# Kernel optimization log

Hardware: AMD Instinct MI355X
Metric: run time of the kernel (lower is better)

The kernel has to match this reference:

```python
import math
import jax, jax.numpy as jnp
import numpy as np

B, C, F, W_FRAMES = 1, 8, 1024, 512
H = 16                      # num_heads
D = F // H                  # head dim = 64
ROPE_DIM = D // 2           # 32: only first half of head dim is rotated
EXP = 4                     # ffn expansion
EPS = 1e-5
MAX_FREQ = 10.0             # rotary-embedding-torch default


def frame_norm(x, g, b):
    # LayerNorm over the feature axis (axis=2) of (b, c, F, w)
    mu = jnp.mean(x, axis=2, keepdims=True)
    var = jnp.mean(jnp.square(x - mu), axis=2, keepdims=True)
    xn = (x - mu) * jax.lax.rsqrt(var + EPS)
    return xn * g[None, None, :, None] + b[None, None, :, None]


def mc_linear(x, w_pw):
    # per-channel pointwise linear: out[b,c,f,w] = sum_g W[c,f,g] x[b,c,g,w]
    return jnp.einsum('bcgw,cfg->bcfw', x, w_pw)


def apply_rope(t, freqs_seq):
    # t: (b, c, H, w, d); freqs_seq: (w, rot_dim)
    rot_dim = freqs_seq.shape[-1]
    t_rot, t_pass = t[..., :rot_dim], t[..., rot_dim:]
    cos, sin = jnp.cos(freqs_seq), jnp.sin(freqs_seq)
    x1, x2 = t_rot[..., 0::2], t_rot[..., 1::2]
    rh = jnp.stack([-x2, x1], axis=-1).reshape(t_rot.shape)  # interleaved rotate_half
    return jnp.concatenate([t_rot * cos + rh * sin, t_pass], axis=-1)


def attention(x, w_q, w_o, rope_freqs):
    b, c, f, w = x.shape
    # NOTE: source uses q_proj for q, k AND v (k_proj/v_proj unused)
    p = mc_linear(x, w_q)                                    # (b,c,F,w)
    t = p.transpose(0, 1, 3, 2).reshape(b, c, w, H, D).transpose(0, 1, 3, 2, 4)  # (b,c,H,w,d)
    pos = jnp.arange(w, dtype=t.dtype)
    freqs_seq = jnp.repeat(pos[:, None] * rope_freqs[None, :], 2, axis=-1)  # (w, rot_dim)
    q = apply_rope(t, freqs_seq)
    k = apply_rope(t, freqs_seq)
    v = t
    scores = jnp.einsum('bchqd,bchkd->bchqk', q, k) / math.sqrt(f)  # scaled by sqrt(features)!
    a = jax.nn.softmax(scores, axis=-1)
    o = jnp.einsum('bchqk,bchkd->bchqd', a, v)
    o = o.transpose(0, 1, 3, 2, 4).reshape(b, c, w, f).transpose(0, 1, 3, 2)  # (b,c,F,w)
    return mc_linear(o, w_o)


def setup_inputs() -> dict:
    key = jax.random.key(0)
    ks = jax.random.split(key, 8)
    s = 1.0 / math.sqrt(F)
    se = 1.0 / math.sqrt(F * EXP)
    x = jax.random.normal(ks[0], (B, C, F, W_FRAMES), dtype=jnp.float32)
    w_q = jax.random.uniform(ks[1], (C, F, F), jnp.float32, -s, s)
    w_o = jax.random.uniform(ks[2], (C, F, F), jnp.float32, -s, s)
    w1 = jax.random.uniform(ks[3], (C, F * EXP, F), jnp.float32, -s, s)
    w2 = jax.random.uniform(ks[4], (C, F, F * EXP), jnp.float32, -se, se)
    rope_freqs = jnp.linspace(1.0, MAX_FREQ / 2, ROPE_DIM // 2, dtype=jnp.float32) * math.pi
    return {
        'x': x,
        'norm1_g': jnp.ones((F,), jnp.float32), 'norm1_b': jnp.zeros((F,), jnp.float32),
        'w_q': w_q, 'w_o': w_o, 'rope_freqs': rope_freqs,
        'norm2_g': jnp.ones((F,), jnp.float32), 'norm2_b': jnp.zeros((F,), jnp.float32),
        'w1': w1, 'w2': w2,
    }


def reference(x, norm1_g, norm1_b, w_q, w_o, rope_freqs, norm2_g, norm2_b, w1, w2):
    # FrameTransformerEncoder, eval mode (dropout = identity)
    z = frame_norm(x, norm1_g, norm1_b)
    x = x + attention(z, w_q, w_o, rope_freqs)
    z = frame_norm(x, norm2_g, norm2_b)
    z = mc_linear(jax.nn.gelu(mc_linear(z, w1), approximate=False), w2)
    return x + z
```

## Files before the change

kernel.cpp:

```cpp
#include <hip/hip_runtime.h>
#include <math.h>

#define CC 8
#define FF 1024
#define WW 512
#define HH 16
#define DD 64
#define FE 4096
#define EPS_ 1e-5f

typedef __attribute__((ext_vector_type(8))) short bf16x8;
typedef __attribute__((ext_vector_type(4))) float f32x4;

static __device__ __forceinline__ unsigned short f2bf(float f) {
    unsigned u = __float_as_uint(f);
    u += 0x7fffu + ((u >> 16) & 1u);
    return (unsigned short)(u >> 16);
}
static __device__ __forceinline__ float bf2f(unsigned short h) {
    return __uint_as_float(((unsigned)h) << 16);
}
static __device__ __forceinline__ float gelu_exact(float v) {
    return 0.5f * v * (1.0f + erff(v * 0.70710678118654752f));
}

typedef const __attribute__((address_space(1))) unsigned int* gas_p;
typedef __attribute__((address_space(3))) unsigned int* las_p;
static __device__ __forceinline__ void gload_lds16(const void* g, void* l) {
    __builtin_amdgcn_global_load_lds((gas_p)g, (las_p)l, 16, 0, 0);
}

__global__ __launch_bounds__(256) void fn_stats_k(
    const float* __restrict__ x, float2* __restrict__ part)
{
    int c  = blockIdx.z;
    int w0 = blockIdx.x * 64;
    int f0 = blockIdx.y * 128;
    int t  = threadIdx.x, wl = t & 63, fg = t >> 6;
    const float* xc = x + (size_t)c * FF * WW;

    float s = 0.f, q = 0.f;
    #pragma unroll 8
    for (int i = 0; i < 32; i++) {
        int f = f0 + fg + 4 * i;
        float v = xc[(size_t)f * WW + w0 + wl];
        s += v; q += v * v;
    }
    __shared__ float ss[4][64], sq_[4][64];
    ss[fg][wl] = s; sq_[fg][wl] = q;
    __syncthreads();
    if (fg == 0) {
        float S = 0.f, Q = 0.f;
        #pragma unroll
        for (int j = 0; j < 4; j++) { S += ss[j][wl]; Q += sq_[j][wl]; }
        part[((size_t)c * WW + w0 + wl) * 8 + blockIdx.y] = make_float2(S, Q);
    }
}

__global__ __launch_bounds__(256) void fn_apply_k(
    const float* __restrict__ x, const float2* __restrict__ part,
    const float* __restrict__ g, const float* __restrict__ b,
    unsigned short* __restrict__ zt)
{
    int c  = blockIdx.z;
    int w0 = blockIdx.x * 64;
    int f0 = blockIdx.y * 64;
    int t  = threadIdx.x, wl = t & 63, fg = t >> 6;

    __shared__ float smu[64], srv[64];
    __shared__ float sT[64][65];

    if (t < 64) {
        float S = 0.f, Q = 0.f;
        #pragma unroll
        for (int fs = 0; fs < 8; fs++) {
            float2 v = part[((size_t)c * WW + w0 + t) * 8 + fs];
            S += v.x; Q += v.y;
        }
        float mu  = S * (1.f / FF);
        float var = Q * (1.f / FF) - mu * mu;
        smu[t] = mu;
        srv[t] = rsqrtf(var + EPS_);
    }
    const float* xc = x + (size_t)c * FF * WW;
    #pragma unroll
    for (int i = 0; i < 16; i++) {
        int fl = fg * 16 + i;
        sT[fl][wl] = xc[(size_t)(f0 + fl) * WW + w0 + wl];
    }
    __syncthreads();

    unsigned short* ztc = zt + (size_t)c * WW * FF;
    float gv = g[f0 + wl], bv = b[f0 + wl];
    #pragma unroll
    for (int i = 0; i < 16; i++) {
        int wr = fg * 16 + i;
        ztc[(size_t)(w0 + wr) * FF + f0 + wl] =
            f2bf((sT[wl][wr] - smu[wr]) * srv[wr] * gv + bv);
    }
}

__global__ __launch_bounds__(256, 3) void gemm_v3_k(
    const float* __restrict__ A, const unsigned short* __restrict__ Bt,
    float* __restrict__ Outf, unsigned short* __restrict__ Outb,
    const float* __restrict__ Add, int M, int K, int mode)
{
    int bid = blockIdx.x;
    int c   = bid & 7;
    int rem = bid >> 3;
    int nt  = rem & 3;
    int mt  = rem >> 2;
    int m0  = mt * 64, n0 = nt * 128;
    const float*          Ac = A  + (size_t)c * M * K;
    const unsigned short* Bc = Bt + ((size_t)c * 512 + n0) * K;

    __shared__ unsigned short sA[2][64 * 72];
    __shared__ unsigned short sB[2][128 * 64];

    int t    = threadIdx.x;
    int lane = t & 63;
    int wid  = t >> 6;
    int frl  = lane & 15, fgr = lane >> 4;
    int WM   = (wid >> 1) * 32, WN = (wid & 1) * 64;

    f32x4 acc[2][4];
    #pragma unroll
    for (int i = 0; i < 2; i++)
        #pragma unroll
        for (int j = 0; j < 4; j++) acc[i][j] = (f32x4){0.f, 0.f, 0.f, 0.f};

    int arow = t >> 4;
    int acol = (t & 15) * 4;
    float4 ar[4];

    int bro   = lane >> 3;
    int bslot = (lane & 7) ^ bro;

    auto loadA = [&](int k0) {
        #pragma unroll
        for (int p = 0; p < 4; p++)
            ar[p] = *reinterpret_cast<const float4*>(
                Ac + (size_t)(m0 + p * 16 + arow) * K + k0 + acol);
    };
    auto writeA = [&](int buf) {
        #pragma unroll
        for (int p = 0; p < 4; p++) {
            ushort4 h;
            h.x = f2bf(ar[p].x); h.y = f2bf(ar[p].y);
            h.z = f2bf(ar[p].z); h.w = f2bf(ar[p].w);
            *reinterpret_cast<ushort4*>(&sA[buf][(p * 16 + arow) * 72 + acol]) = h;
        }
    };
    auto stageB = [&](int buf, int k0) {
        #pragma unroll
        for (int r = 0; r < 4; r++) {
            int rbase = wid * 32 + r * 8;
            gload_lds16(Bc + (size_t)(rbase + bro) * K + k0 + bslot * 8,
                        &sB[buf][rbase * 64]);
        }
    };

    loadA(0);
    stageB(0, 0);
    writeA(0);
    __syncthreads();

    int NT = K >> 6;
    for (int kt = 0; kt < NT; ++kt) {
        int cur = kt & 1;
        if (kt + 1 < NT) {
            loadA((kt + 1) << 6);
            stageB(cur ^ 1, (kt + 1) << 6);
        }
        #pragma unroll
        for (int ks = 0; ks < 2; ks++) {
            bf16x8 af[2], bfv[4];
            #pragma unroll
            for (int mi = 0; mi < 2; mi++)
                af[mi] = *reinterpret_cast<const bf16x8*>(
                    &sA[cur][(WM + mi * 16 + frl) * 72 + ks * 32 + fgr * 8]);
            #pragma unroll
            for (int ni = 0; ni < 4; ni++) {
                int row  = WN + ni * 16 + frl;
                int slot = ((ks << 2) | fgr) ^ (frl & 7);
                bfv[ni] = *reinterpret_cast<const bf16x8*>(
                    &sB[cur][row * 64 + slot * 8]);
            }
            #pragma unroll
            for (int mi = 0; mi < 2; mi++)
                #pragma unroll
                for (int ni = 0; ni < 4; ni++)
                    acc[mi][ni] = __builtin_amdgcn_mfma_f32_16x16x32_bf16(
                        af[mi], bfv[ni], acc[mi][ni], 0, 0, 0);
        }
        if (kt + 1 < NT) writeA(cur ^ 1);
        __syncthreads();
    }

    if (mode == 1) {
        #pragma unroll
        for (int mi = 0; mi < 2; mi++)
            #pragma unroll
            for (int ni = 0; ni < 4; ni++) {
                int mrow = m0 + WM + mi * 16 + fgr * 4;
                int ncol = n0 + WN + ni * 16 + frl;
                #pragma unroll
                for (int r = 0; r < 4; r++) {
                    size_t o = ((size_t)c * M + mrow + r) * 512 + ncol;
                    Outf[o] = acc[mi][ni][r] + Add[o];
                }
            }
    } else {
        bool gel = (mode == 2);
        #pragma unroll
        for (int mi = 0; mi < 2; mi++)
            #pragma unroll
            for (int ni = 0; ni < 4; ni++) {
                f32x4 v = acc[mi][ni];
                if (gel) {
                    v[0] = gelu_exact(v[0]); v[1] = gelu_exact(v[1]);
                    v[2] = gelu_exact(v[2]); v[3] = gelu_exact(v[3]);
                }
                int mrow = m0 + WM + mi * 16 + fgr * 4;
                int ncol = n0 + WN + ni * 16 + frl;
                ushort4 h;
                h.x = f2bf(v[0]); h.y = f2bf(v[1]);
                h.z = f2bf(v[2]); h.w = f2bf(v[3]);
                *reinterpret_cast<ushort4*>(
                    &Outb[((size_t)c * 512 + ncol) * M + mrow]) = h;
            }
    }
}

__global__ __launch_bounds__(256) void attn_mfma_k(
    const unsigned short* __restrict__ pt, const float* __restrict__ fr,
    unsigned short* __restrict__ ot)
{
    int ch = blockIdx.y;
    int c  = ch >> 4, h = ch & 15;
    int q0 = blockIdx.x * 64;
    int t  = threadIdx.x;
    int lane = t & 63;
    int wid  = t >> 6;
    int frl  = lane & 15, fgr = lane >> 4;

    const unsigned short* base = pt + (size_t)c * WW * FF + h * DD;

    __shared__ unsigned short Qs[64 * 72];
    __shared__ unsigned short Ks[64 * 72];
    __shared__ unsigned short Vt[64 * 72];
    __shared__ unsigned short Ps[4 * 16 * 72];

    {
        int kr = t >> 3, d0 = (t & 7) * 8;
        #pragma unroll
        for (int r = 0; r < 2; r++) {
            int row = kr + r * 32;
            int w   = q0 + row;
            bf16x8 v = *reinterpret_cast<const bf16x8*>(&base[(size_t)w * FF + d0]);
            bf16x8 o;
            if (d0 < 32) {
                #pragma unroll
                for (int j = 0; j < 8; j += 2) {
                    float x1 = bf2f((unsigned short)v[j]);
                    float x2 = bf2f((unsigned short)v[j + 1]);
                    float sn, cs;
                    __sincosf((float)w * fr[(d0 + j) >> 1], &sn, &cs);
                    o[j]     = (short)f2bf(x1 * cs - x2 * sn);
                    o[j + 1] = (short)f2bf(x2 * cs + x1 * sn);
                }
            } else o = v;
            *reinterpret_cast<bf16x8*>(&Qs[row * 72 + d0]) = o;
        }
    }

    f32x4 oacc[4];
    float m_[4], l_[4];
    #pragma unroll
    for (int i = 0; i < 4; i++) {
        oacc[i] = (f32x4){0.f, 0.f, 0.f, 0.f};
        m_[i] = -1e30f; l_[i] = 0.f;
    }
    unsigned short* myP = &Ps[wid * 16 * 72];
    int wq0 = wid * 16;

    for (int k0 = 0; k0 < WW; k0 += 64) {
        __syncthreads();
        {
            int kr = t >> 3, d0 = (t & 7) * 8;
            #pragma unroll
            for (int r = 0; r < 2; r++) {
                int row = kr + r * 32;
                int w   = k0 + row;
                bf16x8 v = *reinterpret_cast<const bf16x8*>(&base[(size_t)w * FF + d0]);
                bf16x8 o;
                if (d0 < 32) {
                    #pragma unroll
                    for (int j = 0; j < 8; j += 2) {
                        float x1 = bf2f((unsigned short)v[j]);
                        float x2 = bf2f((unsigned short)v[j + 1]);
                        float sn, cs;
                        __sincosf((float)w * fr[(d0 + j) >> 1], &sn, &cs);
                        o[j]     = (short)f2bf(x1 * cs - x2 * sn);
                        o[j + 1] = (short)f2bf(x2 * cs + x1 * sn);
                    }
                } else o = v;
                *reinterpret_cast<bf16x8*>(&Ks[row * 72 + d0]) = o;
            }
        }
        {
            int d  = t & 63;
            int kb = (t >> 6) * 8;
            #pragma unroll
            for (int r = 0; r < 2; r++) {
                int kk = kb + r * 32;
                bf16x8 o;
                #pragma unroll
                for (int j = 0; j < 8; j++)
                    o[j] = (short)base[(size_t)(k0 + kk + j) * FF + d];
                *reinterpret_cast<bf16x8*>(&Vt[d * 72 + kk]) = o;
            }
        }
        __syncthreads();

        f32x4 s[4];
        #pragma unroll
        for (int nt = 0; nt < 4; nt++) s[nt] = (f32x4){0.f, 0.f, 0.f, 0.f};
        bf16x8 aq0 = *reinterpret_cast<const bf16x8*>(&Qs[(wq0 + frl) * 72 + fgr * 8]);
        bf16x8 aq1 = *reinterpret_cast<const bf16x8*>(&Qs[(wq0 + frl) * 72 + 32 + fgr * 8]);
        #pragma unroll
        for (int nt = 0; nt < 4; nt++) {
            bf16x8 b0 = *reinterpret_cast<const bf16x8*>(&Ks[(nt * 16 + frl) * 72 + fgr * 8]);
            bf16x8 b1 = *reinterpret_cast<const bf16x8*>(&Ks[(nt * 16 + frl) * 72 + 32 + fgr * 8]);
            s[nt] = __builtin_amdgcn_mfma_f32_16x16x32_bf16(aq0, b0, s[nt], 0, 0, 0);
            s[nt] = __builtin_amdgcn_mfma_f32_16x16x32_bf16(aq1, b1, s[nt], 0, 0, 0);
        }

        #pragma unroll
        for (int r = 0; r < 4; r++) {
            float sv[4];
            #pragma unroll
            for (int nt = 0; nt < 4; nt++) sv[nt] = s[nt][r] * (1.f / 32.f);
            float mx = fmaxf(fmaxf(sv[0], sv[1]), fmaxf(sv[2], sv[3]));
            mx = fmaxf(mx, __shfl_xor(mx, 1, 64));
            mx = fmaxf(mx, __shfl_xor(mx, 2, 64));
            mx = fmaxf(mx, __shfl_xor(mx, 4, 64));
            mx = fmaxf(mx, __shfl_xor(mx, 8, 64));
            float mn    = fmaxf(m_[r], mx);
            float scale = __expf(m_[r] - mn);
            float rs = 0.f;
            #pragma unroll
            for (int nt = 0; nt < 4; nt++) {
                float p = __expf(sv[nt] - mn);
                myP[(fgr * 4 + r) * 72 + nt * 16 + frl] = f2bf(p);
                rs += p;
            }
            rs += __shfl_xor(rs, 1, 64);
            rs += __shfl_xor(rs, 2, 64);
            rs += __shfl_xor(rs, 4, 64);
            rs += __shfl_xor(rs, 8, 64);
            l_[r] = l_[r] * scale + rs;
            m_[r] = mn;
            #pragma unroll
            for (int dt = 0; dt < 4; dt++) oacc[dt][r] *= scale;
        }

        bf16x8 ap0 = *reinterpret_cast<const bf16x8*>(&myP[frl * 72 + fgr * 8]);
        bf16x8 ap1 = *reinterpret_cast<const bf16x8*>(&myP[frl * 72 + 32 + fgr * 8]);
        #pragma unroll
        for (int dt = 0; dt < 4; dt++) {
            bf16x8 b0 = *reinterpret_cast<const bf16x8*>(&Vt[(dt * 16 + frl) * 72 + fgr * 8]);
            bf16x8 b1 = *reinterpret_cast<const bf16x8*>(&Vt[(dt * 16 + frl) * 72 + 32 + fgr * 8]);
            oacc[dt] = __builtin_amdgcn_mfma_f32_16x16x32_bf16(ap0, b0, oacc[dt], 0, 0, 0);
            oacc[dt] = __builtin_amdgcn_mfma_f32_16x16x32_bf16(ap1, b1, oacc[dt], 0, 0, 0);
        }
    }

    unsigned short* ob = ot + (size_t)c * WW * FF + h * DD;
    #pragma unroll
    for (int r = 0; r < 4; r++) {
        float inv = 1.f / l_[r];
        int w = q0 + wq0 + fgr * 4 + r;
        #pragma unroll
        for (int dt = 0; dt < 4; dt++)
            ob[(size_t)w * FF + dt * 16 + frl] = f2bf(oacc[dt][r] * inv);
    }
}

extern "C" void kernel_launch(void* const* d_in, const int* in_sizes, int n_in,
                              void* d_out, int out_size, void* d_ws, size_t ws_size,
                              hipStream_t stream)
{
    const float* x  = (const float*)d_in[0];
    const float* g1 = (const float*)d_in[1];
    const float* b1 = (const float*)d_in[2];
    const float* wq = (const float*)d_in[3];
    const float* wo = (const float*)d_in[4];
    const float* fr = (const float*)d_in[5];
    const float* g2 = (const float*)d_in[6];
    const float* b2 = (const float*)d_in[7];
    const float* w1 = (const float*)d_in[8];
    const float* w2 = (const float*)d_in[9];

    const size_t SZ = (size_t)CC * FF * WW;
    char* wsb = (char*)d_ws;
    unsigned short* zt  = (unsigned short*)(wsb);
    unsigned short* ptb = (unsigned short*)(wsb + 2 * SZ);
    unsigned short* otb = (unsigned short*)(wsb + 4 * SZ);
    float*          x2  = (float*)        (wsb + 6 * SZ);
    unsigned short* h1t = (unsigned short*)(wsb + 10 * SZ);
    float2*         prt = (float2*)       (wsb + 18 * SZ);

    dim3 b256(256);
    dim3 gst(WW / 64, FF / 128, CC);
    dim3 gap(WW / 64, FF / 64, CC);

    fn_stats_k<<<gst, b256, 0, stream>>>(x, prt);
    fn_apply_k<<<gap, b256, 0, stream>>>(x, prt, g1, b1, zt);
    gemm_v3_k<<<dim3(8 * 4 * (FF / 64)), b256, 0, stream>>>(
        wq, zt, nullptr, ptb, nullptr, FF, FF, 0);
    attn_mfma_k<<<dim3(WW / 64, CC * HH), b256, 0, stream>>>(ptb, fr, otb);
    gemm_v3_k<<<dim3(8 * 4 * (FF / 64)), b256, 0, stream>>>(
        wo, otb, x2, nullptr, x, FF, FF, 1);
    fn_stats_k<<<gst, b256, 0, stream>>>(x2, prt);
    fn_apply_k<<<gap, b256, 0, stream>>>(x2, prt, g2, b2, zt);
    gemm_v3_k<<<dim3(8 * 4 * (FE / 64)), b256, 0, stream>>>(
        w1, zt, nullptr, h1t, nullptr, FE, FF, 2);
    gemm_v3_k<<<dim3(8 * 4 * (FF / 64)), b256, 0, stream>>>(
        w2, h1t, (float*)d_out, nullptr, x2, FF, FE, 1);
}
```

Before: 282.8 us.

## Deepen GEMM pipeline to prefetch two tiles ahead with explicit waitcnts

Restructures the GEMM main loop so A and B tiles are prefetched two k-steps ahead. A goes through two register buffers and B through a triple-buffered LDS staging area. Fine-grained s_waitcnt vmcnt values and a raw s_barrier replace __syncthreads, and the loop is unrolled by two to alternate the register buffers. fp32-to-bf16 conversion now uses the packed v_cvt_pk_bf16_f32 instruction, and launch bounds drop from 3 to 2 blocks per CU to make room for the extra registers and LDS. The aim is to hide global-load latency behind MFMA work, at the cost of occupancy and fragile hand-counted waitcnt values.

```diff
diff --git a/kernel.cpp b/kernel.cpp
--- a/kernel.cpp
+++ b/kernel.cpp
@@ -22,6 +22,11 @@
 }
 static __device__ __forceinline__ float gelu_exact(float v) {
     return 0.5f * v * (1.0f + erff(v * 0.70710678118654752f));
+}
+static __device__ __forceinline__ unsigned cvt_pk_bf16(float lo, float hi) {
+    unsigned r;
+    asm("v_cvt_pk_bf16_f32 %0, %1, %2" : "=v"(r) : "v"(lo), "v"(hi));
+    return r;
 }
 
 typedef const __attribute__((address_space(1))) unsigned int* gas_p;
@@ -100,11 +105,14 @@
     }
 }
 
-__global__ __launch_bounds__(256, 3) void gemm_v3_k(
+__global__ __launch_bounds__(256, 2) void gemm_v9_k(
     const float* __restrict__ A, const unsigned short* __restrict__ Bt,
     float* __restrict__ Outf, unsigned short* __restrict__ Outb,
     const float* __restrict__ Add, int M, int K, int mode)
 {
+    constexpr int L  = 4;
+    constexpr int AP = 72;
+
     int bid = blockIdx.x;
     int c   = bid & 7;
     int rem = bid >> 3;
@@ -114,8 +122,8 @@
     const float*          Ac = A  + (size_t)c * M * K;
     const unsigned short* Bc = Bt + ((size_t)c * 512 + n0) * K;
 
-    __shared__ unsigned short sA[2][64 * 72];
-    __shared__ unsigned short sB[2][128 * 64];
+    __shared__ unsigned short sA[2][64 * AP];
+    __shared__ unsigned short sB[3][128 * 64];
 
     int t    = threadIdx.x;
     int lane = t & 63;
@@ -131,24 +139,24 @@
 
     int arow = t >> 4;
     int acol = (t & 15) * 4;
-    float4 ar[4];
+    float4 ar0[L], ar1[L];
 
     int bro   = lane >> 3;
     int bslot = (lane & 7) ^ bro;
 
-    auto loadA = [&](int k0) {
-        #pragma unroll
-        for (int p = 0; p < 4; p++)
+    auto loadAinto = [&](int k0, float4 (&ar)[L]) {
+        #pragma unroll
+        for (int p = 0; p < L; p++)
             ar[p] = *reinterpret_cast<const float4*>(
                 Ac + (size_t)(m0 + p * 16 + arow) * K + k0 + acol);
     };
-    auto writeA = [&](int buf) {
-        #pragma unroll
-        for (int p = 0; p < 4; p++) {
-            ushort4 h;
-            h.x = f2bf(ar[p].x); h.y = f2bf(ar[p].y);
-            h.z = f2bf(ar[p].z); h.w = f2bf(ar[p].w);
-            *reinterpret_cast<ushort4*>(&sA[buf][(p * 16 + arow) * 72 + acol]) = h;
+    auto cvtWriteA = [&](int buf, float4 (&ar)[L]) {
+        #pragma unroll
+        for (int p = 0; p < L; p++) {
+            uint2 u;
+            u.x = cvt_pk_bf16(ar[p].x, ar[p].y);
+            u.y = cvt_pk_bf16(ar[p].z, ar[p].w);
+            *reinterpret_cast<uint2*>(&sA[buf][(p * 16 + arow) * AP + acol]) = u;
         }
     };
     auto stageB = [&](int buf, int k0) {
@@ -160,31 +168,44 @@
         }
     };
 
-    loadA(0);
+    int NT = K >> 6;
+
+    loadAinto(0, ar0);
+    asm volatile("s_waitcnt vmcnt(0)" ::: "memory");
+    cvtWriteA(0, ar0);
     stageB(0, 0);
-    writeA(0);
-    __syncthreads();
-
-    int NT = K >> 6;
-    for (int kt = 0; kt < NT; ++kt) {
-        int cur = kt & 1;
-        if (kt + 1 < NT) {
-            loadA((kt + 1) << 6);
-            stageB(cur ^ 1, (kt + 1) << 6);
-        }
+    loadAinto(64, ar1);
+    stageB(1, 64);
+
+    auto body = [&](int kt, float4 (&arW)[L], float4 (&arR)[L]) {
+        int  cur   = kt & 1;
+        bool more1 = (kt + 1 < NT);
+        bool more2 = (kt + 2 < NT);
+
+        if (more1) asm volatile("s_waitcnt vmcnt(8)" ::: "memory");
+        else       asm volatile("s_waitcnt vmcnt(0)" ::: "memory");
+        asm volatile("s_waitcnt lgkmcnt(0)" ::: "memory");
+        __builtin_amdgcn_sched_barrier(0);
+        __builtin_amdgcn_s_barrier();
+
+        if (more2) {
+            loadAinto((kt + 2) << 6, arW);
+            stageB((kt + 2) % 3, (kt + 2) << 6);
+        }
+
         #pragma unroll
         for (int ks = 0; ks < 2; ks++) {
             bf16x8 af[2], bfv[4];
             #pragma unroll
             for (int mi = 0; mi < 2; mi++)
                 af[mi] = *reinterpret_cast<const bf16x8*>(
-                    &sA[cur][(WM + mi * 16 + frl) * 72 + ks * 32 + fgr * 8]);
+                    &sA[cur][(WM + mi * 16 + frl) * AP + ks * 32 + fgr * 8]);
             #pragma unroll
             for (int ni = 0; ni < 4; ni++) {
                 int row  = WN + ni * 16 + frl;
                 int slot = ((ks << 2) | fgr) ^ (frl & 7);
                 bfv[ni] = *reinterpret_cast<const bf16x8*>(
-                    &sB[cur][row * 64 + slot * 8]);
+                    &sB[kt % 3][row * 64 + slot * 8]);
             }
             #pragma unroll
             for (int mi = 0; mi < 2; mi++)
@@ -193,8 +214,18 @@
                     acc[mi][ni] = __builtin_amdgcn_mfma_f32_16x16x32_bf16(
                         af[mi], bfv[ni], acc[mi][ni], 0, 0, 0);
         }
-        if (kt + 1 < NT) writeA(cur ^ 1);
-        __syncthreads();
+
+        if (more1) {
+            if (more2) asm volatile("s_waitcnt vmcnt(12)" ::: "memory");
+            else       asm volatile("s_waitcnt vmcnt(4)" ::: "memory");
+            __builtin_amdgcn_sched_barrier(0);
+            cvtWriteA((kt + 1) & 1, arR);
+        }
+    };
+
+    for (int kt = 0; kt < NT; kt += 2) {
+        body(kt,     ar0, ar1);
+        body(kt + 1, ar1, ar0);
     }
 
     if (mode == 1) {
@@ -417,15 +448,15 @@
 
     fn_stats_k<<<gst, b256, 0, stream>>>(x, prt);
     fn_apply_k<<<gap, b256, 0, stream>>>(x, prt, g1, b1, zt);
-    gemm_v3_k<<<dim3(8 * 4 * (FF / 64)), b256, 0, stream>>>(
+    gemm_v9_k<<<dim3(512), b256, 0, stream>>>(
         wq, zt, nullptr, ptb, nullptr, FF, FF, 0);
     attn_mfma_k<<<dim3(WW / 64, CC * HH), b256, 0, stream>>>(ptb, fr, otb);
-    gemm_v3_k<<<dim3(8 * 4 * (FF / 64)), b256, 0, stream>>>(
+    gemm_v9_k<<<dim3(512), b256, 0, stream>>>(
         wo, otb, x2, nullptr, x, FF, FF, 1);
     fn_stats_k<<<gst, b256, 0, stream>>>(x2, prt);
     fn_apply_k<<<gap, b256, 0, stream>>>(x2, prt, g2, b2, zt);
-    gemm_v3_k<<<dim3(8 * 4 * (FE / 64)), b256, 0, stream>>>(
+    gemm_v9_k<<<dim3(2048), b256, 0, stream>>>(
         w1, zt, nullptr, h1t, nullptr, FE, FF, 2);
-    gemm_v3_k<<<dim3(8 * 4 * (FF / 64)), b256, 0, stream>>>(
+    gemm_v9_k<<<dim3(512), b256, 0, stream>>>(
         w2, h1t, (float*)d_out, nullptr, x2, FF, FE, 1);
 }
```

Result: slower. 296.8 us, median of 2 (+5.0%).
